# Kernel optimization log

Hardware: AMD Instinct MI355X
Metric: run time of the kernel (lower is better)

The kernel has to match this reference:

```python
import jax, jax.numpy as jnp
import numpy as np

B, N, FIN, FOUT, H, U = 2, 2048, 128, 128, 4, 1024
ALPHA = 0.2  # LeakyReLU negative slope
NEG = -9e15  # mask value from the original code


def setup_inputs() -> dict:
    key = jax.random.key(0)
    k0, k1, k2, k3, k4 = jax.random.split(key, 5)
    x = jax.random.normal(k0, (B, N, FIN), dtype=jnp.float32)
    adj = jax.random.randint(k1, (B, N, N), 0, 2, dtype=jnp.int32)
    weights = jax.random.uniform(k2, (B, N - U, U), dtype=jnp.float32)
    # learned params, one per head (xavier-ish scaled normals)
    W = jax.random.normal(k3, (H, FIN, FOUT), dtype=jnp.float32) * 0.05
    a = jax.random.normal(k4, (H, 2 * FOUT, 1), dtype=jnp.float32) * 0.1
    return {"x": x, "weights": weights, "W": W, "a": a, "adj": adj}


def _build_bipartite_weights(weights, n):
    # weights: [B, v, u] -> dense [B, N, N] as in the original cat ops
    b, v, u = weights.shape
    wv = weights[:, :v, :]
    w1 = jnp.concatenate([jnp.zeros((b, u, u), weights.dtype), jnp.swapaxes(wv, 1, 2)], axis=2)  # [B,u,N]
    w2 = jnp.concatenate([wv, jnp.zeros((b, v, v), weights.dtype)], axis=2)                      # [B,v,N]
    return jnp.concatenate([w1, w2], axis=1)  # [B,N,N]


def reference(x, weights, W, a, adj):
    b, n, _ = x.shape
    big_w = _build_bipartite_weights(weights, n)  # [B,N,N]
    mask = adj > 0
    f = W.shape[2]
    outs = []
    for h in range(W.shape[0]):  # small fixed head count
        Wh = x @ W[h]  # [B,N,F]
        a_src = a[h, :f, 0]  # scores decompose: cat([Wh_i, Wh_j]) @ a == Wh_i@a_src + Wh_j@a_dst
        a_dst = a[h, f:, 0]
        e = jax.nn.leaky_relu((Wh @ a_src)[:, :, None] + (Wh @ a_dst)[:, None, :], negative_slope=ALPHA)  # [B,N,N]
        att = jnp.exp(jnp.where(mask, e, NEG)) * big_w
        denom = jnp.clip(jnp.sum(jnp.abs(att), axis=1, keepdims=True), 1e-12, None)  # F.normalize(p=1, dim=1)
        att = att / denom
        outs.append(jax.nn.elu(att @ Wh))  # concat=True head
    return jnp.concatenate(outs, axis=-1)  # [B,N,H*F]
```

## Files before the change

### kernel.cpp

```cpp
#include <hip/hip_runtime.h>
#include <hip/hip_bf16.h>
#include <math.h>

#define BB 2
#define NN 2048
#define FF 128
#define HH 4
#define HALF 1024

typedef __attribute__((ext_vector_type(8))) short short8;
typedef __attribute__((ext_vector_type(4))) short short4v;
typedef __attribute__((ext_vector_type(4))) float f32x4;

__device__ __forceinline__ short f2bf(float f){
    __hip_bfloat16 h = __float2bfloat16(f);
    return *reinterpret_cast<short*>(&h);
}
__device__ __forceinline__ float bf2f(short v){
    __hip_bfloat16 h = *reinterpret_cast<__hip_bfloat16*>(&v);
    return __bfloat162float(h);
}

__global__ __launch_bounds__(256) void k_whmm(const float* __restrict__ x,
        const float* __restrict__ W, const float* __restrict__ a,
        short* __restrict__ WhB, float* __restrict__ sT, float* __restrict__ dT,
        float* __restrict__ denom){
    __shared__ short xs[64 * 136];
    __shared__ short ws_[128 * 130];
    __shared__ float red_s[2][64], red_d[2][64];
    int t = threadIdx.x;
    int w = t >> 6, lane = t & 63;
    int wm = w >> 1, wn = w & 1;
    int n0 = blockIdx.x * 64;
    int h = blockIdx.y, b = blockIdx.z;
    int sl = b * HH + h;
    int flat = blockIdx.x + 32 * (blockIdx.y + HH * blockIdx.z);
    if(t < 64) denom[flat * 64 + t] = 0.f;
    const float* xb = x + ((size_t)b * NN + n0) * FF;
    #pragma unroll
    for(int l = 0; l < 8; l++){
        int flat4 = t + l * 256;
        int row = flat4 >> 5, col4 = flat4 & 31;
        float4 v = *(const float4*)(xb + (size_t)row * FF + col4 * 4);
        short* dst = &xs[row * 136 + col4 * 4];
        dst[0] = f2bf(v.x); dst[1] = f2bf(v.y); dst[2] = f2bf(v.z); dst[3] = f2bf(v.w);
    }
    const float* Wb = W + (size_t)h * FF * FF;
    #pragma unroll
    for(int l = 0; l < 16; l++){
        int flat4 = t + l * 256;
        int row = flat4 >> 5, col4 = flat4 & 31;
        float4 v = *(const float4*)(Wb + (size_t)row * FF + col4 * 4);
        short* dst = &ws_[row * 130 + col4 * 4];
        dst[0] = f2bf(v.x); dst[1] = f2bf(v.y); dst[2] = f2bf(v.z); dst[3] = f2bf(v.w);
    }
    __syncthreads();
    int m = lane & 15, q = lane >> 4;
    f32x4 acc[2][4] = {};
    #pragma unroll
    for(int ks = 0; ks < 4; ks++){
        short8 af[2];
        #pragma unroll
        for(int mi = 0; mi < 2; mi++)
            af[mi] = *(const short8*)&xs[(wm * 32 + mi * 16 + m) * 136 + ks * 32 + q * 8];
        short8 bf[4];
        #pragma unroll
        for(int ni = 0; ni < 4; ni++){
            #pragma unroll
            for(int e = 0; e < 8; e++)
                bf[ni][e] = ws_[(ks * 32 + q * 8 + e) * 130 + wn * 64 + ni * 16 + m];
        }
        #pragma unroll
        for(int mi = 0; mi < 2; mi++)
            #pragma unroll
            for(int ni = 0; ni < 4; ni++)
                acc[mi][ni] = __builtin_amdgcn_mfma_f32_16x16x32_bf16(af[mi], bf[ni], acc[mi][ni], 0, 0, 0);
    }
    float asrc[4], adst[4];
    const float* ah = a + (size_t)h * 2 * FF;
    #pragma unroll
    for(int ni = 0; ni < 4; ni++){
        int col = wn * 64 + ni * 16 + m;
        asrc[ni] = ah[col];
        adst[ni] = ah[FF + col];
    }
    #pragma unroll
    for(int mi = 0; mi < 2; mi++){
        #pragma unroll
        for(int rg = 0; rg < 4; rg++){
            float ps = 0.f, pd = 0.f;
            #pragma unroll
            for(int ni = 0; ni < 4; ni++){
                ps += acc[mi][ni][rg] * asrc[ni];
                pd += acc[mi][ni][rg] * adst[ni];
            }
            #pragma unroll
            for(int msk = 8; msk >= 1; msk >>= 1){
                ps += __shfl_xor(ps, msk);
                pd += __shfl_xor(pd, msk);
            }
            if(m == 0){
                int row = wm * 32 + mi * 16 + q * 4 + rg;
                red_s[wn][row] = ps;
                red_d[wn][row] = pd;
            }
        }
    }
    __syncthreads();
    short* cs = xs;
    #pragma unroll
    for(int mi = 0; mi < 2; mi++){
        #pragma unroll
        for(int ni = 0; ni < 4; ni++){
            int col = wn * 64 + ni * 16 + m;
            #pragma unroll
            for(int rg = 0; rg < 4; rg++){
                int row = wm * 32 + mi * 16 + q * 4 + rg;
                cs[row * 130 + col] = f2bf(acc[mi][ni][rg]);
            }
        }
    }
    if(t < 64){
        int n = n0 + t;
        sT[((size_t)b * NN + n) * HH + h] = red_s[0][t] + red_s[1][t];
        dT[((size_t)b * NN + n) * HH + h] = red_d[0][t] + red_d[1][t];
    }
    __syncthreads();
    #pragma unroll
    for(int fi = 0; fi < 4; fi++){
        int fragId = w * 4 + fi;
        int ktg = fragId >> 3, nt = fragId & 7;
        short8 pk;
        #pragma unroll
        for(int e = 0; e < 8; e++)
            pk[e] = cs[(ktg * 32 + q * 8 + e) * 130 + nt * 16 + m];
        *(short8*)(WhB + (((size_t)sl * 8 + nt) * 64 + blockIdx.x * 2 + ktg) * 512 + lane * 8) = pk;
    }
}

__global__ __launch_bounds__(256) void k_att(const int* __restrict__ adj,
        const float* __restrict__ wv,
        const float* __restrict__ sT, const float* __restrict__ dT,
        short* __restrict__ P, float* __restrict__ denom){
    __shared__ float red[HH][128];
    int t = threadIdx.x;
    int jlane = t & 127, ihalf = t >> 7;
    int jt = blockIdx.x, ic = blockIdx.y, bb = blockIdx.z;
    int b = bb >> 1, blk = bb & 1;
    int jl = jt * 128 + jlane;
    int jg = blk ? jl : HALF + jl;
    int iloc0 = ic * 32 + ihalf * 16;
    int ig0 = (blk ? HALF : 0) + iloc0;
    const int* ap = adj + ((size_t)b * NN + ig0) * NN + jg;
    const float* sp = sT + ((size_t)b * NN + ig0) * HH;
    float4 dv4 = *(const float4*)(dT + ((size_t)b * NN + jg) * HH);
    float da[4] = {dv4.x, dv4.y, dv4.z, dv4.w};
    short* Pp = P + ((size_t)(bb * HH) << 20) + (size_t)iloc0 * 1024 + jl;
    float den[HH] = {};
#define ATTLOOP(WPTR, WSTRIDE) \
    _Pragma("unroll 4") \
    for(int ii = 0; ii < 16; ii++){ \
        int av = ap[(size_t)ii * NN]; \
        float wq = (WPTR)[(size_t)ii * (WSTRIDE)]; \
        float4 s4 = *(const float4*)(sp + ii * HH); \
        float wmv = av > 0 ? wq : 0.f; \
        float sa[4] = {s4.x, s4.y, s4.z, s4.w}; \
        _Pragma("unroll") \
        for(int h = 0; h < HH; h++){ \
            float tt = sa[h] + da[h]; \
            tt = tt > 0.f ? tt : 0.2f * tt; \
            float pe = __expf(tt) * wmv; \
            den[h] += pe; \
            Pp[((size_t)h << 20) + (size_t)ii * 1024] = f2bf(pe); \
        } \
    }
    if(blk){
        const float* wp = wv + ((size_t)b * HALF + iloc0) * HALF + jl;
        ATTLOOP(wp, HALF)
    } else {
        const float* wp = wv + ((size_t)b * HALF + jl) * HALF + iloc0;
        ATTLOOP(wp, 1)
    }
#undef ATTLOOP
    if(ihalf){
        #pragma unroll
        for(int h = 0; h < HH; h++) red[h][jlane] = den[h];
    }
    __syncthreads();
    if(!ihalf){
        #pragma unroll
        for(int h = 0; h < HH; h++)
            atomicAdd(&denom[((size_t)b * HH + h) * NN + jg], den[h] + red[h][jlane]);
    }
}

__global__ __launch_bounds__(256) void k_pv(const short* __restrict__ P,
        const float* __restrict__ denom, const short* __restrict__ WhB,
        float* __restrict__ out){
    __shared__ short lds[2][6656];
    int t = threadIdx.x;
    int w = t >> 6, lane = t & 63;
    int wm = w >> 1, wn = w & 1;
    int mt = blockIdx.x, h = blockIdx.y, bb = blockIdx.z;
    int b = bb >> 1, blk = bb & 1;
    int sl = b * HH + h;
    const short* Prow = P + ((size_t)(bb * HH + h) << 20);
    size_t Bb2 = ((size_t)sl) * 8;
    int koff = blk ? 0 : 32;
    int col0 = blk ? 0 : HALF;
    const float* npb = denom + (size_t)sl * NN + col0;
    int rowA = t >> 3, c8 = t & 7;
    const short* srcA0 = Prow + (size_t)(mt * 32 + rowA) * 1024 + c8 * 4;
    f32x4 acc[4] = {};
    short4v r0; short8 r1, r2; float4 n4;
#define LOADST(KT) { \
    r0 = *(const short4v*)(srcA0 + (KT) * 32); \
    n4 = *(const float4*)(npb + (KT) * 32 + c8 * 4); \
    r1 = *(const short8*)(WhB + ((Bb2 + (t >> 6)) * 64 + koff + (KT)) * 512 + (t & 63) * 8); \
    r2 = *(const short8*)(WhB + ((Bb2 + 4 + (t >> 6)) * 64 + koff + (KT)) * 512 + (t & 63) * 8); }
#define WRITEST(BUF) { \
    short4v rs_; \
    rs_[0] = f2bf(bf2f(r0[0]) * __builtin_amdgcn_rcpf(fmaxf(n4.x, 1e-12f))); \
    rs_[1] = f2bf(bf2f(r0[1]) * __builtin_amdgcn_rcpf(fmaxf(n4.y, 1e-12f))); \
    rs_[2] = f2bf(bf2f(r0[2]) * __builtin_amdgcn_rcpf(fmaxf(n4.z, 1e-12f))); \
    rs_[3] = f2bf(bf2f(r0[3]) * __builtin_amdgcn_rcpf(fmaxf(n4.w, 1e-12f))); \
    *(short4v*)&lds[BUF][rowA * 40 + c8 * 4] = rs_; \
    *(short8*)&lds[BUF][2560 + (t >> 6) * 512 + (t & 63) * 8] = r1; \
    *(short8*)&lds[BUF][2560 + 2048 + (t >> 6) * 512 + (t & 63) * 8] = r2; }
    LOADST(0)
    WRITEST(0)
    __syncthreads();
    int m = lane & 15, q = lane >> 4;
    for(int kt = 0; kt < 32; kt++){
        int cur = kt & 1;
        if(kt < 31){ LOADST(kt + 1) }
        short8 af = *(const short8*)&lds[cur][(wm * 16 + m) * 40 + q * 8];
        short8 bf[4];
        #pragma unroll
        for(int ni = 0; ni < 4; ni++)
            bf[ni] = *(const short8*)&lds[cur][2560 + (wn * 4 + ni) * 512 + lane * 8];
        #pragma unroll
        for(int ni = 0; ni < 4; ni++)
            acc[ni] = __builtin_amdgcn_mfma_f32_16x16x32_bf16(af, bf[ni], acc[ni], 0, 0, 0);
        __syncthreads();
        if(kt < 31){
            WRITEST(cur ^ 1)
            __syncthreads();
        }
    }
    int rq = lane >> 4, rc = lane & 15;
    int rowg0 = (blk ? HALF : 0) + mt * 32 + wm * 16;
    #pragma unroll
    for(int ni = 0; ni < 4; ni++){
        int f = (wn * 4 + ni) * 16 + rc;
        #pragma unroll
        for(int rg = 0; rg < 4; rg++){
            float v = acc[ni][rg];
            v = v > 0.f ? v : expm1f(v);
            out[((size_t)b * NN + rowg0 + rq * 4 + rg) * (HH * FF) + h * FF + f] = v;
        }
    }
#undef LOADST
#undef WRITEST
}

extern "C" void kernel_launch(void* const* d_in, const int* in_sizes, int n_in,
                              void* d_out, int out_size, void* d_ws, size_t ws_size,
                              hipStream_t stream){
    const float* x   = (const float*)d_in[0];
    const float* wv  = (const float*)d_in[1];
    const float* W   = (const float*)d_in[2];
    const float* a   = (const float*)d_in[3];
    const int*   adj = (const int*)d_in[4];
    float* out = (float*)d_out;

    char* ws = (char*)d_ws;
    short* P     = (short*)ws;
    short* WhB   = (short*)(ws + 33554432);
    float* sT    = (float*)(ws + 37748736);
    float* dT    = (float*)(ws + 37814272);
    float* denom = (float*)(ws + 37879808);

    k_whmm<<<dim3(32, HH, BB), 256, 0, stream>>>(x, W, a, WhB, sT, dT, denom);
    k_att<<<dim3(8, 32, 4), 256, 0, stream>>>(adj, wv, sT, dT, P, denom);
    k_pv<<<dim3(32, HH, 4), 256, 0, stream>>>(P, denom, WhB, out);
}
```

Baseline: 47.90 us.

## Vectorize attention kernel with 4x4 register tiles and precompute inverse norms in LDS

Measured after the change: 63.92 us. 1.33x slower.

```diff
diff --git a/kernel.cpp b/kernel.cpp
--- a/kernel.cpp
+++ b/kernel.cpp
@@ -142,55 +142,79 @@
         const float* __restrict__ wv,
         const float* __restrict__ sT, const float* __restrict__ dT,
         short* __restrict__ P, float* __restrict__ denom){
-    __shared__ float red[HH][128];
+    __shared__ float red[3][64][17];
     int t = threadIdx.x;
-    int jlane = t & 127, ihalf = t >> 7;
+    int jlane = t & 63, irow = t >> 6;
     int jt = blockIdx.x, ic = blockIdx.y, bb = blockIdx.z;
     int b = bb >> 1, blk = bb & 1;
-    int jl = jt * 128 + jlane;
-    int jg = blk ? jl : HALF + jl;
-    int iloc0 = ic * 32 + ihalf * 16;
-    int ig0 = (blk ? HALF : 0) + iloc0;
-    const int* ap = adj + ((size_t)b * NN + ig0) * NN + jg;
-    const float* sp = sT + ((size_t)b * NN + ig0) * HH;
-    float4 dv4 = *(const float4*)(dT + ((size_t)b * NN + jg) * HH);
-    float da[4] = {dv4.x, dv4.y, dv4.z, dv4.w};
-    short* Pp = P + ((size_t)(bb * HH) << 20) + (size_t)iloc0 * 1024 + jl;
-    float den[HH] = {};
-#define ATTLOOP(WPTR, WSTRIDE) \
-    _Pragma("unroll 4") \
-    for(int ii = 0; ii < 16; ii++){ \
-        int av = ap[(size_t)ii * NN]; \
-        float wq = (WPTR)[(size_t)ii * (WSTRIDE)]; \
-        float4 s4 = *(const float4*)(sp + ii * HH); \
-        float wmv = av > 0 ? wq : 0.f; \
-        float sa[4] = {s4.x, s4.y, s4.z, s4.w}; \
-        _Pragma("unroll") \
-        for(int h = 0; h < HH; h++){ \
-            float tt = sa[h] + da[h]; \
-            tt = tt > 0.f ? tt : 0.2f * tt; \
-            float pe = __expf(tt) * wmv; \
-            den[h] += pe; \
-            Pp[((size_t)h << 20) + (size_t)ii * 1024] = f2bf(pe); \
-        } \
-    }
+    int jl4 = jt * 256 + jlane * 4;
+    int jg4 = (blk ? 0 : HALF) + jl4;
+    int il0 = ic * 16 + irow * 4;
+    int ig0 = (blk ? HALF : 0) + il0;
+    float dreg[4][4];
+    #pragma unroll
+    for(int e = 0; e < 4; e++){
+        float4 d4 = *(const float4*)(dT + ((size_t)b * NN + jg4 + e) * HH);
+        dreg[e][0]=d4.x; dreg[e][1]=d4.y; dreg[e][2]=d4.z; dreg[e][3]=d4.w;
+    }
+    float wvr[4][4];
     if(blk){
-        const float* wp = wv + ((size_t)b * HALF + iloc0) * HALF + jl;
-        ATTLOOP(wp, HALF)
+        #pragma unroll
+        for(int r = 0; r < 4; r++){
+            float4 w4 = *(const float4*)(wv + ((size_t)b * HALF + il0 + r) * HALF + jl4);
+            wvr[r][0]=w4.x; wvr[r][1]=w4.y; wvr[r][2]=w4.z; wvr[r][3]=w4.w;
+        }
     } else {
-        const float* wp = wv + ((size_t)b * HALF + jl) * HALF + iloc0;
-        ATTLOOP(wp, 1)
-    }
-#undef ATTLOOP
-    if(ihalf){
-        #pragma unroll
-        for(int h = 0; h < HH; h++) red[h][jlane] = den[h];
-    }
-    __syncthreads();
-    if(!ihalf){
-        #pragma unroll
-        for(int h = 0; h < HH; h++)
-            atomicAdd(&denom[((size_t)b * HH + h) * NN + jg], den[h] + red[h][jlane]);
+        #pragma unroll
+        for(int e = 0; e < 4; e++){
+            float4 w4 = *(const float4*)(wv + ((size_t)b * HALF + jl4 + e) * HALF + il0);
+            wvr[0][e]=w4.x; wvr[1][e]=w4.y; wvr[2][e]=w4.z; wvr[3][e]=w4.w;
+        }
+    }
+    const int* apb = adj + ((size_t)b * NN + ig0) * NN + jg4;
+    short* Pp = P + ((size_t)(bb * HH) << 20) + (size_t)il0 * 1024 + jl4;
+    float den[4][4] = {};
+    #pragma unroll
+    for(int r = 0; r < 4; r++){
+        int4 a4 = *(const int4*)(apb + (size_t)r * NN);
+        int aa[4] = {a4.x, a4.y, a4.z, a4.w};
+        float4 s4 = *(const float4*)(sT + ((size_t)b * NN + ig0 + r) * HH);
+        float sa[4] = {s4.x, s4.y, s4.z, s4.w};
+        float wm[4];
+        #pragma unroll
+        for(int e = 0; e < 4; e++) wm[e] = aa[e] > 0 ? wvr[r][e] : 0.f;
+        #pragma unroll
+        for(int h = 0; h < 4; h++){
+            short4v pk;
+            #pragma unroll
+            for(int e = 0; e < 4; e++){
+                float tt = sa[h] + dreg[e][h];
+                tt = tt > 0.f ? tt : 0.2f * tt;
+                float pe = __expf(tt) * wm[e];
+                den[h][e] += pe;
+                pk[e] = f2bf(pe);
+            }
+            *(short4v*)(Pp + ((size_t)h << 20) + (size_t)r * 1024) = pk;
+        }
+    }
+    if(irow){
+        #pragma unroll
+        for(int h = 0; h < 4; h++)
+            #pragma unroll
+            for(int e = 0; e < 4; e++)
+                red[irow - 1][jlane][h * 4 + e] = den[h][e];
+    }
+    __syncthreads();
+    if(!irow){
+        #pragma unroll
+        for(int h = 0; h < 4; h++){
+            #pragma unroll
+            for(int e = 0; e < 4; e++){
+                int idx = h * 4 + e;
+                float v = den[h][e] + red[0][jlane][idx] + red[1][jlane][idx] + red[2][jlane][idx];
+                atomicAdd(&denom[((size_t)b * HH + h) * NN + jg4 + e], v);
+            }
+        }
     }
 }
 
@@ -198,6 +222,7 @@
         const float* __restrict__ denom, const short* __restrict__ WhB,
         float* __restrict__ out){
     __shared__ short lds[2][6656];
+    __shared__ float invs[1024];
     int t = threadIdx.x;
     int w = t >> 6, lane = t & 63;
     int wm = w >> 1, wn = w & 1;
@@ -209,24 +234,30 @@
     int koff = blk ? 0 : 32;
     int col0 = blk ? 0 : HALF;
     const float* npb = denom + (size_t)sl * NN + col0;
+    #pragma unroll
+    for(int l = 0; l < 4; l++){
+        int j = t + l * 256;
+        invs[j] = __builtin_amdgcn_rcpf(fmaxf(npb[j], 1e-12f));
+    }
     int rowA = t >> 3, c8 = t & 7;
     const short* srcA0 = Prow + (size_t)(mt * 32 + rowA) * 1024 + c8 * 4;
     f32x4 acc[4] = {};
-    short4v r0; short8 r1, r2; float4 n4;
+    short4v r0; short8 r1, r2; float4 iv4;
 #define LOADST(KT) { \
     r0 = *(const short4v*)(srcA0 + (KT) * 32); \
-    n4 = *(const float4*)(npb + (KT) * 32 + c8 * 4); \
+    iv4 = *(const float4*)&invs[(KT) * 32 + c8 * 4]; \
     r1 = *(const short8*)(WhB + ((Bb2 + (t >> 6)) * 64 + koff + (KT)) * 512 + (t & 63) * 8); \
     r2 = *(const short8*)(WhB + ((Bb2 + 4 + (t >> 6)) * 64 + koff + (KT)) * 512 + (t & 63) * 8); }
 #define WRITEST(BUF) { \
     short4v rs_; \
-    rs_[0] = f2bf(bf2f(r0[0]) * __builtin_amdgcn_rcpf(fmaxf(n4.x, 1e-12f))); \
-    rs_[1] = f2bf(bf2f(r0[1]) * __builtin_amdgcn_rcpf(fmaxf(n4.y, 1e-12f))); \
-    rs_[2] = f2bf(bf2f(r0[2]) * __builtin_amdgcn_rcpf(fmaxf(n4.z, 1e-12f))); \
-    rs_[3] = f2bf(bf2f(r0[3]) * __builtin_amdgcn_rcpf(fmaxf(n4.w, 1e-12f))); \
+    rs_[0] = f2bf(bf2f(r0[0]) * iv4.x); \
+    rs_[1] = f2bf(bf2f(r0[1]) * iv4.y); \
+    rs_[2] = f2bf(bf2f(r0[2]) * iv4.z); \
+    rs_[3] = f2bf(bf2f(r0[3]) * iv4.w); \
     *(short4v*)&lds[BUF][rowA * 40 + c8 * 4] = rs_; \
     *(short8*)&lds[BUF][2560 + (t >> 6) * 512 + (t & 63) * 8] = r1; \
     *(short8*)&lds[BUF][2560 + 2048 + (t >> 6) * 512 + (t & 63) * 8] = r2; }
+    __syncthreads();
     LOADST(0)
     WRITEST(0)
     __syncthreads();
@@ -282,6 +313,6 @@
     float* denom = (float*)(ws + 37879808);
 
     k_whmm<<<dim3(32, HH, BB), 256, 0, stream>>>(x, W, a, WhB, sT, dT, denom);
-    k_att<<<dim3(8, 32, 4), 256, 0, stream>>>(adj, wv, sT, dT, P, denom);
+    k_att<<<dim3(4, 64, 4), 256, 0, stream>>>(adj, wv, sT, dT, P, denom);
     k_pv<<<dim3(32, HH, 4), 256, 0, stream>>>(P, denom, WhB, out);
 }
```
